# Kernel tuning notes

Hardware: AMD Instinct MI355X
Metric: run time of the kernel (lower is better)

Reference implementation:

```python
import jax, jax.numpy as jnp
import numpy as np

B, T, D_IN, D, K, H, BAND = 4, 1536, 512, 512, 2, 8, 24
DH = D // H
ALPHA, BETA, EPS = 6.0, 0.5, 1e-5


def _ln(x, g, b):
    m = x.mean(-1, keepdims=True)
    v = ((x - m) ** 2).mean(-1, keepdims=True)
    return (x - m) / jnp.sqrt(v + EPS) * g + b


def setup_inputs() -> dict:
    key = jax.random.key(0)
    ks = jax.random.split(key, 16)
    sc = 0.02
    inp = {
        "x_m": jax.random.normal(ks[0], (B, T, D_IN), jnp.float32),
        "A": jax.random.uniform(ks[1], (B, T, K), jnp.float32),
        "W_in": jax.random.normal(ks[2], (D_IN, D), jnp.float32) * sc,
        "b_in": jnp.zeros((D,), jnp.float32),
        "ln_q_g": jnp.ones((D,), jnp.float32), "ln_q_b": jnp.zeros((D,), jnp.float32),
        "ln_kv_g": jnp.ones((D,), jnp.float32), "ln_kv_b": jnp.zeros((D,), jnp.float32),
        "Wq": jax.random.normal(ks[3], (D, D), jnp.float32) * sc,
        "bq": jnp.zeros((D,), jnp.float32),
        "Wk": jax.random.normal(ks[4], (D, D), jnp.float32) * sc,
        "bk": jnp.zeros((D,), jnp.float32),
        "Wv": jax.random.normal(ks[5], (D, D), jnp.float32) * sc,
        "bv": jnp.zeros((D,), jnp.float32),
        "Wo": jax.random.normal(ks[6], (D, D), jnp.float32) * sc,
        "bo": jnp.zeros((D,), jnp.float32),
        "ln_f_g": jnp.ones((D,), jnp.float32), "ln_f_b": jnp.zeros((D,), jnp.float32),
        "W1": jax.random.normal(ks[7], (D, 4 * D), jnp.float32) * sc,
        "b1": jnp.zeros((4 * D,), jnp.float32),
        "W2": jax.random.normal(ks[8], (4 * D, D), jnp.float32) * sc,
        "b2": jnp.zeros((D,), jnp.float32),
        "ln_s_g": jnp.ones((D,), jnp.float32), "ln_s_b": jnp.zeros((D,), jnp.float32),
        "spk_tags": jax.random.normal(ks[9], (K, D), jnp.float32) / np.sqrt(D),
    }
    return inp


def reference(x_m, A, W_in, b_in, ln_q_g, ln_q_b, ln_kv_g, ln_kv_b,
              Wq, bq, Wk, bk, Wv, bv, Wo, bo,
              ln_f_g, ln_f_b, W1, b1, W2, b2, ln_s_g, ln_s_b, spk_tags):
    X = x_m @ W_in + b_in                      # [B,T,D]
    W_hat = jax.nn.sigmoid(ALPHA * (A - BETA))  # [B,T,K] sigmoid gating

    # banded additive mask (|i-j| <= BAND allowed)
    idx = jnp.arange(T)
    allowed = jnp.abs(idx[:, None] - idx[None, :]) <= BAND
    mask = jnp.where(allowed, 0.0, -jnp.inf).astype(X.dtype)  # [T,T]

    # K/V come from the (shared) mixed memory X
    KV = _ln(X, ln_kv_g, ln_kv_b)
    k_p = (KV @ Wk + bk).reshape(B, T, H, DH)
    v_p = (KV @ Wv + bv).reshape(B, T, H, DH)

    streams = []
    for kk in range(K):
        Xk = X * W_hat[..., kk:kk + 1]
        Q = _ln(Xk, ln_q_g, ln_q_b)
        q = (Q @ Wq + bq).reshape(B, T, H, DH)
        scores = jnp.einsum('bthd,bshd->bhts', q, k_p) / np.sqrt(DH) + mask
        p = jax.nn.softmax(scores, axis=-1)
        y = jnp.einsum('bhts,bshd->bthd', p, v_p).reshape(B, T, D) @ Wo + bo
        y = Xk + y                              # residual after attention
        h = _ln(y, ln_f_g, ln_f_b)
        h = jax.nn.gelu(h @ W1 + b1, approximate=False) @ W2 + b2
        out_k = y + h + spk_tags[kk]            # ffn residual + speaker tag
        out_k = _ln(out_k, ln_s_g, ln_s_b)      # per-stream LayerNorm
        streams.append(out_k)
    return jnp.concatenate(streams, axis=1)    # [B, K*T, D]
```

## Files before the change

### kernel.cpp

```cpp
#include <hip/hip_runtime.h>
#include <hip/hip_bf16.h>
#include <math.h>

#define B_    4
#define T_    1536
#define DIN_  512
#define D_    512
#define K_    2
#define H_    8
#define BAND_ 24
#define DH_   64
#define M_    (B_*T_)
#define M2_   (2*M_)
#define ALPHA_ 6.0f
#define BETA_  0.5f
#define EPS_   1e-5f

using bf8  = __attribute__((ext_vector_type(8))) short;
using f32x4 = __attribute__((ext_vector_type(4))) float;

__device__ __forceinline__ void async_copy16(const void* g, void* l) {
  __builtin_amdgcn_global_load_lds(
      (const __attribute__((address_space(1))) unsigned int*)g,
      (__attribute__((address_space(3))) unsigned int*)l, 16, 0, 0);
}

__device__ __forceinline__ short f2bf(float v) {
  __hip_bfloat16 h = (__hip_bfloat16)v;
  return *(short*)&h;
}
__device__ __forceinline__ float bf2f(short s) {
  union { unsigned u; float f; } c;
  c.u = ((unsigned)(unsigned short)s) << 16;
  return c.f;
}
__device__ __forceinline__ int swz64(int row, int col) {
  return (col & ~63) | ((((col >> 3) ^ row) & 7) << 3) | (col & 7);
}
__device__ __forceinline__ float fast_gelu(float x) {
  const float t = fmaf(0.1029504013f, x * x, 2.3021170686f);
  const float e = __builtin_amdgcn_exp2f(x * t);
  const float r = __builtin_amdgcn_rcpf(e + 1.0f);
  return fmaf(-x, r, x);
}
__device__ __forceinline__ float wave_sum(float s) {
#pragma unroll
  for (int o = 1; o < 64; o <<= 1) s += __shfl_xor(s, o);
  return s;
}

template<int BM, int BN, int NI, int NJ, int FLAGS>
__global__ __launch_bounds__(256) void gemm_bt_t(
    const short* __restrict__ A, const short* __restrict__ Bt,
    const float* __restrict__ bias, const void* __restrict__ res,
    const float* __restrict__ tag2,
    void* __restrict__ Cout, int M, int N, int Kd, int gx) {
  __shared__ short lA[BM * 64];
  __shared__ short lB[BN * 64];
  const int gy   = gridDim.x / gx;
  const int xcd  = blockIdx.x & 7;
  const int seq  = blockIdx.x >> 3;
  const int rpx  = gy >> 3;
  const int by   = xcd * rpx + seq / gx;
  const int bx   = seq % gx;
  const int tid  = threadIdx.x;
  const int wave = tid >> 6, lane = tid & 63;
  const int block_m = by * BM, block_n = bx * BN;
  const int wm = (wave & 1) * (BM / 2), wn = (wave >> 1) * (BN / 2);
  const int l15 = lane & 15, quad = lane >> 4, l7 = lane & 7;
  f32x4 acc[NI][NJ] = {};

  for (int k0 = 0; k0 < Kd; k0 += 64) {
    __syncthreads();
#pragma unroll
    for (int i = 0; i < BM / 32; ++i) {
      const int cb = wave * (BM * 2) + i * 64;
      const int c  = cb + lane;
      async_copy16(A + (size_t)(block_m + (c >> 3)) * Kd + k0 + (c & 7) * 8,
                   &lA[cb * 8]);
    }
#pragma unroll
    for (int i = 0; i < BN / 32; ++i) {
      const int cb = wave * (BN * 2) + i * 64;
      const int c  = cb + lane;
      async_copy16(Bt + (size_t)(block_n + (c >> 3)) * Kd + k0 + (c & 7) * 8,
                   &lB[cb * 8]);
    }
    __syncthreads();
#pragma unroll
    for (int ks = 0; ks < 2; ++ks) {
      bf8 af[NI], bfr[NJ];
#pragma unroll
      for (int i = 0; i < NI; ++i)
        af[i] = *(const bf8*)&lA[(wm + i * 16 + l15) * 64 + (((ks * 4 + quad) ^ l7) << 3)];
#pragma unroll
      for (int j = 0; j < NJ; ++j)
        bfr[j] = *(const bf8*)&lB[(wn + j * 16 + l15) * 64 + (((ks * 4 + quad) ^ l7) << 3)];
#pragma unroll
      for (int i = 0; i < NI; ++i)
#pragma unroll
        for (int j = 0; j < NJ; ++j)
          acc[i][j] = __builtin_amdgcn_mfma_f32_16x16x32_bf16(bfr[j], af[i], acc[i][j], 0, 0, 0);
    }
  }

  const int half = M >> 1;
#pragma unroll
  for (int i = 0; i < NI; ++i) {
    const int row  = block_m + wm + i * 16 + l15;
    const size_t rowN = (size_t)row * N;
    const int toff = (row >= half) ? N : 0;
#pragma unroll
    for (int j = 0; j < NJ; ++j) {
      const int colb = block_n + wn + j * 16 + quad * 4;
      const float4 bb = *(const float4*)&bias[colb];
      float v0 = acc[i][j][0] + bb.x;
      float v1 = acc[i][j][1] + bb.y;
      float v2 = acc[i][j][2] + bb.z;
      float v3 = acc[i][j][3] + bb.w;
      if constexpr (FLAGS & 8) {
        const short4 rv = *(const short4*)&((const short*)res)[rowN + colb];
        v0 += bf2f(rv.x); v1 += bf2f(rv.y); v2 += bf2f(rv.z); v3 += bf2f(rv.w);
      }
      if constexpr (FLAGS & 16) {
        const float4 rv = *(const float4*)&((const float*)res)[rowN + colb];
        v0 += rv.x; v1 += rv.y; v2 += rv.z; v3 += rv.w;
      }
      if constexpr (FLAGS & 32) {
        const float4 tg = *(const float4*)&tag2[toff + colb];
        v0 += tg.x; v1 += tg.y; v2 += tg.z; v3 += tg.w;
      }
      if constexpr (FLAGS & 1) {
        v0 = fast_gelu(v0); v1 = fast_gelu(v1);
        v2 = fast_gelu(v2); v3 = fast_gelu(v3);
      }
      if constexpr (FLAGS & 2) {
        const int oc = (FLAGS & 4) ? swz64(row, colb) : colb;
        short4 o;
        o.x = f2bf(v0); o.y = f2bf(v1); o.z = f2bf(v2); o.w = f2bf(v3);
        *(short4*)&((short*)Cout)[rowN + oc] = o;
      } else {
        float4 o; o.x = v0; o.y = v1; o.z = v2; o.w = v3;
        *(float4*)&((float*)Cout)[rowN + colb] = o;
      }
    }
  }
}

__device__ __forceinline__ void gemm128_core(
    const short* __restrict__ A, const short* __restrict__ Bt,
    const float* __restrict__ bias, short* __restrict__ Cout,
    int N, int Kd, int bid, int gx, int gy, short* lA, short* lB) {
  const int xcd  = bid & 7;
  const int seq  = bid >> 3;
  const int rpx  = gy >> 3;
  const int by   = xcd * rpx + seq / gx;
  const int bx   = seq % gx;
  const int tid  = threadIdx.x;
  const int wave = tid >> 6, lane = tid & 63;
  const int block_m = by * 128, block_n = bx * 128;
  const int wm = (wave & 1) * 64, wn = (wave >> 1) * 64;
  const int l15 = lane & 15, quad = lane >> 4, l7 = lane & 7;
  f32x4 acc[4][4] = {};

  for (int k0 = 0; k0 < Kd; k0 += 64) {
    __syncthreads();
#pragma unroll
    for (int i = 0; i < 4; ++i) {
      const int cb = wave * 256 + i * 64;
      const int c  = cb + lane;
      async_copy16(A + (size_t)(block_m + (c >> 3)) * Kd + k0 + (c & 7) * 8,
                   &lA[cb * 8]);
    }
#pragma unroll
    for (int i = 0; i < 4; ++i) {
      const int cb = wave * 256 + i * 64;
      const int c  = cb + lane;
      async_copy16(Bt + (size_t)(block_n + (c >> 3)) * Kd + k0 + (c & 7) * 8,
                   &lB[cb * 8]);
    }
    __syncthreads();
#pragma unroll
    for (int ks = 0; ks < 2; ++ks) {
      bf8 af[4], bfr[4];
#pragma unroll
      for (int i = 0; i < 4; ++i)
        af[i] = *(const bf8*)&lA[(wm + i * 16 + l15) * 64 + (((ks * 4 + quad) ^ l7) << 3)];
#pragma unroll
      for (int j = 0; j < 4; ++j)
        bfr[j] = *(const bf8*)&lB[(wn + j * 16 + l15) * 64 + (((ks * 4 + quad) ^ l7) << 3)];
#pragma unroll
      for (int i = 0; i < 4; ++i)
#pragma unroll
        for (int j = 0; j < 4; ++j)
          acc[i][j] = __builtin_amdgcn_mfma_f32_16x16x32_bf16(bfr[j], af[i], acc[i][j], 0, 0, 0);
    }
  }

#pragma unroll
  for (int i = 0; i < 4; ++i) {
    const int row  = block_m + wm + i * 16 + l15;
    const size_t rowN = (size_t)row * N;
#pragma unroll
    for (int j = 0; j < 4; ++j) {
      const int colb = block_n + wn + j * 16 + quad * 4;
      const float4 bb = *(const float4*)&bias[colb];
      short4 o;
      o.x = f2bf(acc[i][j][0] + bb.x);
      o.y = f2bf(acc[i][j][1] + bb.y);
      o.z = f2bf(acc[i][j][2] + bb.z);
      o.w = f2bf(acc[i][j][3] + bb.w);
      *(short4*)&Cout[rowN + colb] = o;
    }
  }
}

__global__ __launch_bounds__(256) void gemm_dual_k(
    const short* __restrict__ A0, const short* __restrict__ Bt0,
    const float* __restrict__ bias0, short* __restrict__ C0, int N0, int nb0, int gx0,
    const short* __restrict__ A1, const short* __restrict__ Bt1,
    const float* __restrict__ bias1, short* __restrict__ C1, int N1, int gx1) {
  __shared__ short lA[128 * 64];
  __shared__ short lB[128 * 64];
  const int bid = blockIdx.x;
  if (bid < nb0) {
    gemm128_core(A0, Bt0, bias0, C0, N0, D_, bid, gx0, nb0 / gx0, lA, lB);
  } else {
    const int b1 = bid - nb0;
    const int nb1 = gridDim.x - nb0;
    gemm128_core(A1, Bt1, bias1, C1, N1, D_, b1, gx1, nb1 / gx1, lA, lB);
  }
}

__device__ __forceinline__ void tconv_tile(const float* __restrict__ W,
                                           short* __restrict__ Wt, int K, int N,
                                           int bx, int by, int tid, float (*s)[33]) {
  const int tx = tid & 31, ty = tid >> 5;
  const int k0 = by * 32, n0 = bx * 32;
#pragma unroll
  for (int r = 0; r < 4; ++r)
    s[ty * 4 + r][tx] = W[(size_t)(k0 + ty * 4 + r) * N + n0 + tx];
  __syncthreads();
#pragma unroll
  for (int r = 0; r < 4; ++r) {
    const int n = n0 + ty * 4 + r;
    Wt[(size_t)n * K + swz64(n, k0 + tx)] = f2bf(s[tx][ty * 4 + r]);
  }
}

__global__ __launch_bounds__(256) void prep_k(
    const float* __restrict__ x_m, short* __restrict__ xb,
    const float* __restrict__ W_in, short* __restrict__ WtIn,
    const float* __restrict__ Wq,  short* __restrict__ WtQ,
    const float* __restrict__ Wk,  const float* __restrict__ Wv,
    short* __restrict__ WtKV,
    const float* __restrict__ Wo,  short* __restrict__ WtO,
    const float* __restrict__ W1,  short* __restrict__ Wt1,
    const float* __restrict__ W2,  short* __restrict__ Wt2,
    const float* __restrict__ bk,  const float* __restrict__ bv,
    float* __restrict__ bkv) {
  __shared__ float s[32][33];
  const int blk = blockIdx.x, tid = threadIdx.x;
  if (blk < 3072) {
    const int e = (blk * 256 + tid) * 4;
    const int row = e >> 9, col = e & 511;
    const float4 v = *(const float4*)&x_m[e];
    short4 o;
    o.x = f2bf(v.x); o.y = f2bf(v.y); o.z = f2bf(v.z); o.w = f2bf(v.w);
    *(short4*)&xb[((size_t)row << 9) | swz64(row, col)] = o;
  } else if (blk < 3328) {
    const int t = blk - 3072; tconv_tile(W_in, WtIn, DIN_, D_, t & 15, t >> 4, tid, s);
  } else if (blk < 3584) {
    const int t = blk - 3328; tconv_tile(Wq, WtQ, D_, D_, t & 15, t >> 4, tid, s);
  } else if (blk < 3840) {
    const int t = blk - 3584; tconv_tile(Wk, WtKV, D_, D_, t & 15, t >> 4, tid, s);
  } else if (blk < 4096) {
    const int t = blk - 3840; tconv_tile(Wv, WtKV + (size_t)D_ * D_, D_, D_, t & 15, t >> 4, tid, s);
  } else if (blk < 4352) {
    const int t = blk - 4096; tconv_tile(Wo, WtO, D_, D_, t & 15, t >> 4, tid, s);
  } else if (blk < 5376) {
    const int t = blk - 4352; tconv_tile(W1, Wt1, D_, 4 * D_, t & 63, t >> 6, tid, s);
  } else if (blk < 6400) {
    const int t = blk - 5376; tconv_tile(W2, Wt2, 4 * D_, D_, t & 15, t >> 4, tid, s);
  } else {
    const int i = (blk - 6400) * 256 + tid;
    bkv[i] = (i < D_) ? bk[i] : bv[i - D_];
  }
}

__global__ __launch_bounds__(256) void ln_bf_k(const short* __restrict__ in,
                                               const float* __restrict__ g,
                                               const float* __restrict__ b,
                                               short* __restrict__ out) {
  const int row  = blockIdx.x * 4 + (threadIdx.x >> 6);
  const int lane = threadIdx.x & 63;
  const int c0   = lane * 8;
  const bf8 xv = *(const bf8*)&in[(size_t)row * D_ + c0];
  float v[8];
  float s = 0.0f;
#pragma unroll
  for (int e = 0; e < 8; ++e) { v[e] = bf2f(xv[e]); s += v[e]; }
  const float mean = wave_sum(s) * (1.0f / D_);
  float s2 = 0.0f;
#pragma unroll
  for (int e = 0; e < 8; ++e) { v[e] -= mean; s2 += v[e] * v[e]; }
  const float inv = rsqrtf(wave_sum(s2) * (1.0f / D_) + EPS_);
  const float4 g0 = *(const float4*)&g[c0];
  const float4 g1 = *(const float4*)&g[c0 + 4];
  const float4 b0 = *(const float4*)&b[c0];
  const float4 b1 = *(const float4*)&b[c0 + 4];
  bf8 o;
  o[0] = f2bf(v[0] * inv * g0.x + b0.x);
  o[1] = f2bf(v[1] * inv * g0.y + b0.y);
  o[2] = f2bf(v[2] * inv * g0.z + b0.z);
  o[3] = f2bf(v[3] * inv * g0.w + b0.w);
  o[4] = f2bf(v[4] * inv * g1.x + b1.x);
  o[5] = f2bf(v[5] * inv * g1.y + b1.y);
  o[6] = f2bf(v[6] * inv * g1.z + b1.z);
  o[7] = f2bf(v[7] * inv * g1.w + b1.w);
  *(bf8*)&out[(size_t)row * D_ + swz64(row, c0)] = o;
}

__global__ __launch_bounds__(256) void ln_gate_k(
    const short* __restrict__ X, const float* __restrict__ Ain,
    const float* __restrict__ gkv, const float* __restrict__ bkvp,
    const float* __restrict__ gq, const float* __restrict__ bqp,
    short* __restrict__ KVb, short* __restrict__ Xk, short* __restrict__ LNq) {
  const int row  = blockIdx.x * 4 + (threadIdx.x >> 6);
  const int lane = threadIdx.x & 63;
  const int c0   = lane * 8;
  float v[8];
  float s = 0.0f;
  if (row < M_) {
    const bf8 xv = *(const bf8*)&X[(size_t)row * D_ + c0];
#pragma unroll
    for (int e = 0; e < 8; ++e) { v[e] = bf2f(xv[e]); s += v[e]; }
    const float mean = wave_sum(s) * (1.0f / D_);
    float s2 = 0.0f;
#pragma unroll
    for (int e = 0; e < 8; ++e) { v[e] -= mean; s2 += v[e] * v[e]; }
    const float inv = rsqrtf(wave_sum(s2) * (1.0f / D_) + EPS_);
    const float4 g0 = *(const float4*)&gkv[c0];
    const float4 g1 = *(const float4*)&gkv[c0 + 4];
    const float4 b0 = *(const float4*)&bkvp[c0];
    const float4 b1 = *(const float4*)&bkvp[c0 + 4];
    bf8 o;
    o[0] = f2bf(v[0] * inv * g0.x + b0.x);
    o[1] = f2bf(v[1] * inv * g0.y + b0.y);
    o[2] = f2bf(v[2] * inv * g0.z + b0.z);
    o[3] = f2bf(v[3] * inv * g0.w + b0.w);
    o[4] = f2bf(v[4] * inv * g1.x + b1.x);
    o[5] = f2bf(v[5] * inv * g1.y + b1.y);
    o[6] = f2bf(v[6] * inv * g1.z + b1.z);
    o[7] = f2bf(v[7] * inv * g1.w + b1.w);
    *(bf8*)&KVb[(size_t)row * D_ + swz64(row, c0)] = o;
  } else {
    const int r2 = row - M_;
    const int kk = r2 / M_, rm = r2 % M_;
    const float a = Ain[(size_t)rm * K_ + kk];
    const float w = __builtin_amdgcn_rcpf(1.0f + __expf(-ALPHA_ * (a - BETA_)));
    const bf8 xv = *(const bf8*)&X[(size_t)rm * D_ + c0];
    bf8 xo;
#pragma unroll
    for (int e = 0; e < 8; ++e) {
      v[e] = bf2f(xv[e]) * w;
      xo[e] = f2bf(v[e]);
      s += v[e];
    }
    *(bf8*)&Xk[(size_t)r2 * D_ + c0] = xo;
    const float mean = wave_sum(s) * (1.0f / D_);
    float s2 = 0.0f;
#pragma unroll
    for (int e = 0; e < 8; ++e) { v[e] -= mean; s2 += v[e] * v[e]; }
    const float inv = rsqrtf(wave_sum(s2) * (1.0f / D_) + EPS_);
    const float4 g0 = *(const float4*)&gq[c0];
    const float4 g1 = *(const float4*)&gq[c0 + 4];
    const float4 b0 = *(const float4*)&bqp[c0];
    const float4 b1 = *(const float4*)&bqp[c0 + 4];
    bf8 o;
    o[0] = f2bf(v[0] * inv * g0.x + b0.x);
    o[1] = f2bf(v[1] * inv * g0.y + b0.y);
    o[2] = f2bf(v[2] * inv * g0.z + b0.z);
    o[3] = f2bf(v[3] * inv * g0.w + b0.w);
    o[4] = f2bf(v[4] * inv * g1.x + b1.x);
    o[5] = f2bf(v[5] * inv * g1.y + b1.y);
    o[6] = f2bf(v[6] * inv * g1.z + b1.z);
    o[7] = f2bf(v[7] * inv * g1.w + b1.w);
    *(bf8*)&LNq[(size_t)r2 * D_ + swz64(r2, c0)] = o;
  }
}

__global__ __launch_bounds__(256) void final_ln_k(
    const short* __restrict__ t2, const float* __restrict__ g,
    const float* __restrict__ b, float* __restrict__ out) {
  const int row  = blockIdx.x * 4 + (threadIdx.x >> 6);
  const int lane = threadIdx.x & 63;
  const int c0   = lane * 8;
  const int kk = row / M_, rm = row % M_;
  const int bb_ = rm / T_, t = rm % T_;
  const size_t orow = (size_t)bb_ * (K_ * T_) + (size_t)kk * T_ + t;
  const bf8 xv = *(const bf8*)&t2[(size_t)row * D_ + c0];
  float v[8];
  float s = 0.0f;
#pragma unroll
  for (int e = 0; e < 8; ++e) { v[e] = bf2f(xv[e]); s += v[e]; }
  const float mean = wave_sum(s) * (1.0f / D_);
  float s2 = 0.0f;
#pragma unroll
  for (int e = 0; e < 8; ++e) { v[e] -= mean; s2 += v[e] * v[e]; }
  const float inv = rsqrtf(wave_sum(s2) * (1.0f / D_) + EPS_);
  const float4 g0 = *(const float4*)&g[c0];
  const float4 g1 = *(const float4*)&g[c0 + 4];
  const float4 b0 = *(const float4*)&b[c0];
  const float4 b1 = *(const float4*)&b[c0 + 4];
  float4 o0, o1;
  o0.x = v[0] * inv * g0.x + b0.x;
  o0.y = v[1] * inv * g0.y + b0.y;
  o0.z = v[2] * inv * g0.z + b0.z;
  o0.w = v[3] * inv * g0.w + b0.w;
  o1.x = v[4] * inv * g1.x + b1.x;
  o1.y = v[5] * inv * g1.y + b1.y;
  o1.z = v[6] * inv * g1.z + b1.z;
  o1.w = v[7] * inv * g1.w + b1.w;
  *(float4*)&out[orow * D_ + c0]     = o0;
  *(float4*)&out[orow * D_ + c0 + 4] = o1;
}

#define QT_  64
#define KT_  (QT_ + 2 * BAND_)
#define SKQ_ 72
#define STV_ 136
__global__ __launch_bounds__(256) void attn_mfma_k(
    const short* __restrict__ q, const short* __restrict__ KVp,
    short* __restrict__ out) {
  __shared__ short sK[KT_ * SKQ_];
  __shared__ short sQ[QT_ * SKQ_];
  __shared__ short sVt[DH_ * STV_];
  __shared__ short sP[4][16 * SKQ_];
  const int t0 = blockIdx.x * QT_;
  const int h  = blockIdx.y;
  const int z  = blockIdx.z;
  const int b  = z % B_;
  const int tid = threadIdx.x;
  const int wave = tid >> 6, lane = tid & 63;
  const int rr = tid >> 5, c2 = tid & 31;

  for (int r0 = 0; r0 < KT_; r0 += 8) {
    const int r = r0 + rr;
    const int s = t0 - BAND_ + r;
    short2 kv = {0, 0}, vv = {0, 0};
    if (s >= 0 && s < T_) {
      const size_t g = (size_t)(b * T_ + s) * (2 * D_) + h * DH_ + c2 * 2;
      kv = *(const short2*)&KVp[g];
      vv = *(const short2*)&KVp[g + D_];
    }
    *(short2*)&sK[r * SKQ_ + c2 * 2] = kv;
    sVt[(c2 * 2)     * STV_ + r] = vv.x;
    sVt[(c2 * 2 + 1) * STV_ + r] = vv.y;
  }
  for (int r0 = 0; r0 < QT_; r0 += 8) {
    const int r = r0 + rr;
    const size_t g = (size_t)(z * T_ + t0 + r) * D_ + h * DH_ + c2 * 2;
    *(short2*)&sQ[r * SKQ_ + c2 * 2] = *(const short2*)&q[g];
  }
  __syncthreads();

  const int qg  = wave * 16;
  const int l15 = lane & 15, quad = lane >> 4;

  bf8 qa0 = *(const bf8*)&sQ[(qg + l15) * SKQ_ + quad * 8];
  bf8 qa1 = *(const bf8*)&sQ[(qg + l15) * SKQ_ + 32 + quad * 8];
  f32x4 acc[4];
#pragma unroll
  for (int j = 0; j < 4; ++j) {
    const bf8 kb0 = *(const bf8*)&sK[(qg + j * 16 + l15) * SKQ_ + quad * 8];
    const bf8 kb1 = *(const bf8*)&sK[(qg + j * 16 + l15) * SKQ_ + 32 + quad * 8];
    f32x4 z4 = {0.f, 0.f, 0.f, 0.f};
    acc[j] = __builtin_amdgcn_mfma_f32_16x16x32_bf16(qa0, kb0, z4, 0, 0, 0);
    acc[j] = __builtin_amdgcn_mfma_f32_16x16x32_bf16(qa1, kb1, acc[j], 0, 0, 0);
  }

#pragma unroll
  for (int reg = 0; reg < 4; ++reg) {
    const int i = quad * 4 + reg;
    float sc[4];
    float mx = -1e30f;
#pragma unroll
    for (int j = 0; j < 4; ++j) {
      const int c = j * 16 + l15;
      const int s = t0 + qg - BAND_ + c;
      const int rel = c - i;
      const bool valid = (rel >= 0) && (rel <= 2 * BAND_) && (s >= 0) && (s < T_);
      sc[j] = valid ? acc[j][reg] * 0.125f : -1e30f;
      mx = fmaxf(mx, sc[j]);
    }
    for (int o = 1; o < 16; o <<= 1) mx = fmaxf(mx, __shfl_xor(mx, o));
    float p[4], se = 0.0f;
#pragma unroll
    for (int j = 0; j < 4; ++j) {
      p[j] = (sc[j] > -1e29f) ? __expf(sc[j] - mx) : 0.0f;
      se += p[j];
    }
    for (int o = 1; o < 16; o <<= 1) se += __shfl_xor(se, o);
    const float inv = __builtin_amdgcn_rcpf(se);
#pragma unroll
    for (int j = 0; j < 4; ++j)
      sP[wave][i * SKQ_ + j * 16 + l15] = f2bf(p[j] * inv);
  }

  const bf8 pa0 = *(const bf8*)&sP[wave][l15 * SKQ_ + quad * 8];
  const bf8 pa1 = *(const bf8*)&sP[wave][l15 * SKQ_ + 32 + quad * 8];
  f32x4 oacc[4] = {};
#pragma unroll
  for (int dt = 0; dt < 4; ++dt) {
    const bf8 vb0 = *(const bf8*)&sVt[(dt * 16 + l15) * STV_ + qg + quad * 8];
    const bf8 vb1 = *(const bf8*)&sVt[(dt * 16 + l15) * STV_ + qg + 32 + quad * 8];
    oacc[dt] = __builtin_amdgcn_mfma_f32_16x16x32_bf16(pa0, vb0, oacc[dt], 0, 0, 0);
    oacc[dt] = __builtin_amdgcn_mfma_f32_16x16x32_bf16(pa1, vb1, oacc[dt], 0, 0, 0);
  }
#pragma unroll
  for (int dt = 0; dt < 4; ++dt)
#pragma unroll
    for (int reg = 0; reg < 4; ++reg) {
      const int i = quad * 4 + reg;
      const int row = t0 + qg + i;
      const int col = h * DH_ + dt * 16 + l15;
      out[(size_t)(z * T_ + row) * D_ + swz64(row, col)] = f2bf(oacc[dt][reg]);
    }
}

extern "C" void kernel_launch(void* const* d_in, const int* in_sizes, int n_in,
                              void* d_out, int out_size, void* d_ws, size_t ws_size,
                              hipStream_t stream) {
  const float* x_m    = (const float*)d_in[0];
  const float* A      = (const float*)d_in[1];
  const float* W_in   = (const float*)d_in[2];
  const float* b_in   = (const float*)d_in[3];
  const float* ln_q_g = (const float*)d_in[4];
  const float* ln_q_b = (const float*)d_in[5];
  const float* ln_kv_g= (const float*)d_in[6];
  const float* ln_kv_b= (const float*)d_in[7];
  const float* Wq     = (const float*)d_in[8];
  const float* bq     = (const float*)d_in[9];
  const float* Wk     = (const float*)d_in[10];
  const float* bk     = (const float*)d_in[11];
  const float* Wv     = (const float*)d_in[12];
  const float* bv     = (const float*)d_in[13];
  const float* Wo     = (const float*)d_in[14];
  const float* bo     = (const float*)d_in[15];
  const float* ln_f_g = (const float*)d_in[16];
  const float* ln_f_b = (const float*)d_in[17];
  const float* W1     = (const float*)d_in[18];
  const float* b1     = (const float*)d_in[19];
  const float* W2     = (const float*)d_in[20];
  const float* b2     = (const float*)d_in[21];
  const float* ln_s_g = (const float*)d_in[22];
  const float* ln_s_b = (const float*)d_in[23];
  const float* tags   = (const float*)d_in[24];
  float* out = (float*)d_out;

  const size_t MD = (size_t)M_ * D_;
  float* bkv = (float*)d_ws;
  short* X    = (short*)(bkv + 1024);
  short* Xk2  = X    + MD;
  short* LNb2 = Xk2  + 2 * MD;
  short* qb2  = LNb2 + 2 * MD;
  short* KVpb = qb2  + 2 * MD;
  short* T2b  = KVpb + 2 * MD;
  short* H1b  = T2b  + 2 * MD;
  short* WtIn = H1b + (size_t)M2_ * 4 * D_;
  short* WtQ  = WtIn + (size_t)D_ * DIN_;
  short* WtKV = WtQ  + (size_t)D_ * D_;
  short* WtO  = WtKV + (size_t)2 * D_ * D_;
  short* Wt1  = WtO  + (size_t)D_ * D_;
  short* Wt2  = Wt1  + (size_t)4 * D_ * D_;
  short* KVb  = Wt2  + (size_t)4 * D_ * D_;
  short* xb   = qb2;

  prep_k<<<6404, 256, 0, stream>>>(x_m, xb, W_in, WtIn, Wq, WtQ, Wk, Wv, WtKV,
                                   Wo, WtO, W1, Wt1, W2, Wt2, bk, bv, bkv);

  gemm_bt_t<128,64,4,2, 2><<<(D_/64) * (M_/128), 256, 0, stream>>>(
      xb, WtIn, b_in, nullptr, nullptr, X, M_, D_, DIN_, D_/64);

  ln_gate_k<<<(3 * M_) / 4, 256, 0, stream>>>(
      X, A, ln_kv_g, ln_kv_b, ln_q_g, ln_q_b, KVb, Xk2, LNb2);

  gemm_dual_k<<<768, 256, 0, stream>>>(
      KVb, WtKV, bkv, KVpb, 2 * D_, ((2*D_)/128) * (M_/128), (2*D_)/128,
      LNb2, WtQ, bq, qb2, D_, D_/128);

  attn_mfma_k<<<dim3(T_/QT_, H_, B_*K_), 256, 0, stream>>>(qb2, KVpb, LNb2);
  gemm_bt_t<128,128,4,4, 2|8><<<(D_/128) * (M2_/128), 256, 0, stream>>>(
      LNb2, WtO, bo, Xk2, nullptr, Xk2, M2_, D_, D_, D_/128);
  ln_bf_k<<<M2_/4, 256, 0, stream>>>(Xk2, ln_f_g, ln_f_b, LNb2);
  gemm_bt_t<128,128,4,4, 1|2|4><<<((4*D_)/128) * (M2_/128), 256, 0, stream>>>(
      LNb2, Wt1, b1, nullptr, nullptr, H1b, M2_, 4*D_, D_, (4*D_)/128);
  gemm_bt_t<128,64,4,2, 2|8|32><<<(D_/64) * (M2_/128), 256, 0, stream>>>(
      H1b, Wt2, b2, Xk2, tags, T2b, M2_, D_, 4*D_, D_/64);
  final_ln_k<<<M2_/4, 256, 0, stream>>>(T2b, ln_s_g, ln_s_b, out);
}
```

Baseline: 302.7 us.

## Double-buffer LDS tiles in GEMM kernels to overlap loads with MFMA

Converts the GEMM main loops in the templated GEMM and the dual 128x128 GEMM core to a two-stage LDS ping-pong. The next K tile is issued via async global-to-LDS copies before computing on the current tile, with one barrier per iteration instead of two. This aims to hide global load latency behind MFMA work. It doubles shared memory per block, which can lower occupancy.

```diff
diff --git a/kernel.cpp b/kernel.cpp
--- a/kernel.cpp
+++ b/kernel.cpp
@@ -55,8 +55,8 @@
     const float* __restrict__ bias, const void* __restrict__ res,
     const float* __restrict__ tag2,
     void* __restrict__ Cout, int M, int N, int Kd, int gx) {
-  __shared__ short lA[BM * 64];
-  __shared__ short lB[BN * 64];
+  __shared__ short lA[2][BM * 64];
+  __shared__ short lB[2][BN * 64];
   const int gy   = gridDim.x / gx;
   const int xcd  = blockIdx.x & 7;
   const int seq  = blockIdx.x >> 3;
@@ -70,39 +70,50 @@
   const int l15 = lane & 15, quad = lane >> 4, l7 = lane & 7;
   f32x4 acc[NI][NJ] = {};
 
-  for (int k0 = 0; k0 < Kd; k0 += 64) {
-    __syncthreads();
+  auto stage = [&](int buf, int k0) {
 #pragma unroll
     for (int i = 0; i < BM / 32; ++i) {
       const int cb = wave * (BM * 2) + i * 64;
       const int c  = cb + lane;
       async_copy16(A + (size_t)(block_m + (c >> 3)) * Kd + k0 + (c & 7) * 8,
-                   &lA[cb * 8]);
+                   &lA[buf][cb * 8]);
     }
 #pragma unroll
     for (int i = 0; i < BN / 32; ++i) {
       const int cb = wave * (BN * 2) + i * 64;
       const int c  = cb + lane;
       async_copy16(Bt + (size_t)(block_n + (c >> 3)) * Kd + k0 + (c & 7) * 8,
-                   &lB[cb * 8]);
-    }
-    __syncthreads();
+                   &lB[buf][cb * 8]);
+    }
+  };
+  auto compute = [&](int buf) {
 #pragma unroll
     for (int ks = 0; ks < 2; ++ks) {
       bf8 af[NI], bfr[NJ];
 #pragma unroll
       for (int i = 0; i < NI; ++i)
-        af[i] = *(const bf8*)&lA[(wm + i * 16 + l15) * 64 + (((ks * 4 + quad) ^ l7) << 3)];
+        af[i] = *(const bf8*)&lA[buf][(wm + i * 16 + l15) * 64 + (((ks * 4 + quad) ^ l7) << 3)];
 #pragma unroll
       for (int j = 0; j < NJ; ++j)
-        bfr[j] = *(const bf8*)&lB[(wn + j * 16 + l15) * 64 + (((ks * 4 + quad) ^ l7) << 3)];
+        bfr[j] = *(const bf8*)&lB[buf][(wn + j * 16 + l15) * 64 + (((ks * 4 + quad) ^ l7) << 3)];
 #pragma unroll
       for (int i = 0; i < NI; ++i)
 #pragma unroll
         for (int j = 0; j < NJ; ++j)
           acc[i][j] = __builtin_amdgcn_mfma_f32_16x16x32_bf16(bfr[j], af[i], acc[i][j], 0, 0, 0);
     }
-  }
+  };
+
+  stage(0, 0);
+  __syncthreads();
+  int cur = 0;
+  for (int k0 = 64; k0 < Kd; k0 += 64) {
+    stage(cur ^ 1, k0);
+    compute(cur);
+    __syncthreads();
+    cur ^= 1;
+  }
+  compute(cur);
 
   const int half = M >> 1;
 #pragma unroll
@@ -150,7 +161,7 @@
 __device__ __forceinline__ void gemm128_core(
     const short* __restrict__ A, const short* __restrict__ Bt,
     const float* __restrict__ bias, short* __restrict__ Cout,
-    int N, int Kd, int bid, int gx, int gy, short* lA, short* lB) {
+    int N, int Kd, int bid, int gx, int gy, short (*lA)[128 * 64], short (*lB)[128 * 64]) {
   const int xcd  = bid & 7;
   const int seq  = bid >> 3;
   const int rpx  = gy >> 3;
@@ -163,39 +174,50 @@
   const int l15 = lane & 15, quad = lane >> 4, l7 = lane & 7;
   f32x4 acc[4][4] = {};
 
-  for (int k0 = 0; k0 < Kd; k0 += 64) {
-    __syncthreads();
+  auto stage = [&](int buf, int k0) {
 #pragma unroll
     for (int i = 0; i < 4; ++i) {
       const int cb = wave * 256 + i * 64;
       const int c  = cb + lane;
       async_copy16(A + (size_t)(block_m + (c >> 3)) * Kd + k0 + (c & 7) * 8,
-                   &lA[cb * 8]);
+                   &lA[buf][cb * 8]);
     }
 #pragma unroll
     for (int i = 0; i < 4; ++i) {
       const int cb = wave * 256 + i * 64;
       const int c  = cb + lane;
       async_copy16(Bt + (size_t)(block_n + (c >> 3)) * Kd + k0 + (c & 7) * 8,
-                   &lB[cb * 8]);
-    }
-    __syncthreads();
+                   &lB[buf][cb * 8]);
+    }
+  };
+  auto compute = [&](int buf) {
 #pragma unroll
     for (int ks = 0; ks < 2; ++ks) {
       bf8 af[4], bfr[4];
 #pragma unroll
       for (int i = 0; i < 4; ++i)
-        af[i] = *(const bf8*)&lA[(wm + i * 16 + l15) * 64 + (((ks * 4 + quad) ^ l7) << 3)];
+        af[i] = *(const bf8*)&lA[buf][(wm + i * 16 + l15) * 64 + (((ks * 4 + quad) ^ l7) << 3)];
 #pragma unroll
       for (int j = 0; j < 4; ++j)
-        bfr[j] = *(const bf8*)&lB[(wn + j * 16 + l15) * 64 + (((ks * 4 + quad) ^ l7) << 3)];
+        bfr[j] = *(const bf8*)&lB[buf][(wn + j * 16 + l15) * 64 + (((ks * 4 + quad) ^ l7) << 3)];
 #pragma unroll
       for (int i = 0; i < 4; ++i)
 #pragma unroll
         for (int j = 0; j < 4; ++j)
           acc[i][j] = __builtin_amdgcn_mfma_f32_16x16x32_bf16(bfr[j], af[i], acc[i][j], 0, 0, 0);
     }
-  }
+  };
+
+  stage(0, 0);
+  __syncthreads();
+  int cur = 0;
+  for (int k0 = 64; k0 < Kd; k0 += 64) {
+    stage(cur ^ 1, k0);
+    compute(cur);
+    __syncthreads();
+    cur ^= 1;
+  }
+  compute(cur);
 
 #pragma unroll
   for (int i = 0; i < 4; ++i) {
@@ -220,8 +242,8 @@
     const float* __restrict__ bias0, short* __restrict__ C0, int N0, int nb0, int gx0,
     const short* __restrict__ A1, const short* __restrict__ Bt1,
     const float* __restrict__ bias1, short* __restrict__ C1, int N1, int gx1) {
-  __shared__ short lA[128 * 64];
-  __shared__ short lB[128 * 64];
+  __shared__ short lA[2][128 * 64];
+  __shared__ short lB[2][128 * 64];
   const int bid = blockIdx.x;
   if (bid < nb0) {
     gemm128_core(A0, Bt0, bias0, C0, N0, D_, bid, gx0, nb0 / gx0, lA, lB);
```

Measured after the change: 310.5 us. 2.6% more time.
